# Kernel tuning notes

Hardware: AMD Instinct MI355X
Metric: run time of the kernel (lower is better)

## Reference

```python
import jax, jax.numpy as jnp
import numpy as np

B, N, D, H = 256, 1000, 128, 8
DH = D // H
TANH_CLIP = 10.0
NEG = -1e9  # finite stand-in for -inf mask fill (keeps grads clean)


def setup_inputs() -> dict:
    key = jax.random.key(0)
    ks = jax.random.split(key, 8)
    s = 1.0 / np.sqrt(D)
    return {
        "node_embeddings": jax.random.normal(ks[0], (B, N, D), jnp.float32),
        "W_node": jax.random.normal(ks[1], (D, 3 * D), jnp.float32) * s,   # project_node_embeddings
        "W_fixed": jax.random.normal(ks[2], (D, D), jnp.float32) * s,      # project_fixed_context
        "W_step": jax.random.normal(ks[3], (2 * D, D), jnp.float32) * s,   # project_step_context
        "W_out": jax.random.normal(ks[4], (D, D), jnp.float32) * s,        # project_out
        "prev_idx": jax.random.randint(ks[5], (B,), 0, N),
        "first_idx": jax.random.randint(ks[6], (B,), 0, N),
        "mask": jax.random.randint(ks[7], (B, N), 0, 2).astype(bool),      # True = masked/visited
    }


def reference(node_embeddings, W_node, W_fixed, W_step, W_out, prev_idx, first_idx, mask):
    b = jnp.arange(B)
    # Precompute fixed: context projection of graph embedding (mean aggregation)
    graph_embed = node_embeddings.mean(axis=1)                    # (B, D)
    fixed_context = graph_embed @ W_fixed                          # (B, D)
    # glimpse key / glimpse val / logit key from node embeddings
    kvl = node_embeddings @ W_node                                 # (B, N, 3D)
    glimpse_K, glimpse_V, logit_K = jnp.split(kvl, 3, axis=-1)
    gK = glimpse_K.reshape(B, N, H, DH)                            # (B, N, H, dh)
    gV = glimpse_V.reshape(B, N, H, DH)
    # Step context: cat(first node embed, last node embed) -> query
    step_ctx = jnp.concatenate(
        [node_embeddings[b, first_idx], node_embeddings[b, prev_idx]], axis=-1)  # (B, 2D)
    query = fixed_context + step_ctx @ W_step                      # (B, D)
    Q = query.reshape(B, H, DH)                                    # (B, H, dh)
    # Glimpse MHA (single query per batch element)
    compat = jnp.einsum("bhd,bnhd->bhn", Q, gK) / np.sqrt(DH)      # (B, H, N)
    compat = jnp.where(mask[:, None, :], NEG, compat)              # mask_inner
    attn = jax.nn.softmax(compat, axis=-1)
    heads = jnp.einsum("bhn,bnhd->bhd", attn, gV)                  # (B, H, dh)
    glimpse = heads.reshape(B, D) @ W_out                          # (B, D)
    # Logits against logit_K, tanh clipping, mask_logits, log-softmax
    logits = jnp.einsum("bd,bnd->bn", glimpse, logit_K) / np.sqrt(D)
    logits = TANH_CLIP * jnp.tanh(logits)
    logits = jnp.where(mask, NEG, logits)
    log_p = jax.nn.log_softmax(logits, axis=-1)                    # (B, N)
    return log_p
```

## Files before the change

### kernel.cpp

```cpp
#include <hip/hip_runtime.h>
#include <math.h>

#define BB 256
#define NN 1000
#define DD 128
#define HH 8
#define QQ 4
#define RQ 250
#define NEG -1e9f

#define SY_CNTA 0
#define SY_QK   1
#define SY_CNTC 2
#define SY_GQ   3
#define SY_CNTE 4

__device__ __forceinline__ bool get_mask(const void* m, int flag, size_t idx) {
    if (flag == 1) return ((const int*)m)[idx] != 0;
    if (flag == 2) return ((const float*)m)[idx] != 0.0f;
    return ((const unsigned char*)m)[idx] != 0;
}

__device__ __forceinline__ void sy_arrive(int* p) {
    __builtin_amdgcn_fence(__ATOMIC_RELEASE, "agent");
    __hip_atomic_fetch_add(p, 1, __ATOMIC_RELAXED, __HIP_MEMORY_SCOPE_AGENT);
}
__device__ __forceinline__ void sy_set(int* p) {
    __builtin_amdgcn_fence(__ATOMIC_RELEASE, "agent");
    __hip_atomic_store(p, 1, __ATOMIC_RELAXED, __HIP_MEMORY_SCOPE_AGENT);
}
__device__ __forceinline__ void sy_wait(int* p, int tgt) {
    while (__hip_atomic_load(p, __ATOMIC_RELAXED, __HIP_MEMORY_SCOPE_AGENT) < tgt)
        __builtin_amdgcn_s_sleep(8);
    __builtin_amdgcn_fence(__ATOMIC_ACQUIRE, "agent");
}

__global__ __launch_bounds__(256, 4) void k_one(
        const float* __restrict__ X, const float* __restrict__ Wnode,
        const float* __restrict__ Wfix, const float* __restrict__ Wstep,
        const float* __restrict__ Wout, const int* __restrict__ prev,
        const int* __restrict__ first, const void* __restrict__ mask,
        int* __restrict__ syg, float* __restrict__ partial,
        float* __restrict__ qkg, float* __restrict__ sqw,
        float* __restrict__ pvp, float* __restrict__ gqg,
        float* __restrict__ esumg, float* __restrict__ out) {
    const int bid = blockIdx.x, tid = threadIdx.x;
    const int b = bid >> 2, q = bid & 3;
    const int n0 = q * RQ;
    const size_t xoff = (size_t)b * NN * DD;
    int* sy = syg + b * 16;

    __shared__ __align__(16) unsigned char pool[16384];
    __shared__ __align__(16) float qks[HH][DD];
    __shared__ float gqv[DD];
    __shared__ float lgl[256];
    __shared__ unsigned short cidxL[256];
    __shared__ float redS[4][HH];
    __shared__ float Sh[HH];
    __shared__ float redw[4];
    __shared__ int wbase[4];
    __shared__ int s_flag, s_cnt;
    float* poolf = (float*)pool;

    if (tid < 64) {
        const unsigned int* mw = (const unsigned int*)mask;
        unsigned int a0 = mw[tid], a1 = mw[tid + 64], a2 = mw[tid + 128], a3 = mw[tid + 192];
        int ii = (a0 <= 1u) && (a1 <= 1u) && (a2 <= 1u) && (a3 <= 1u);
        int ff = (a0 == 0u || a0 == 0x3F800000u) && (a1 == 0u || a1 == 0x3F800000u) &&
                 (a2 == 0u || a2 == 0x3F800000u) && (a3 == 0u || a3 == 0x3F800000u);
        int ai = __all(ii), af = __all(ff);
        if (tid == 0) s_flag = ai ? 1 : (af ? 2 : 0);
    }

    {
        float4* red4 = (float4*)pool;
        int c = tid & 31, s = tid >> 5;
        const float4* Xr = (const float4*)(X + xoff);
        float4 acc = make_float4(0.f, 0.f, 0.f, 0.f);
        for (int nl = s; nl < RQ; nl += 8) {
            float4 v = Xr[(n0 + nl) * 32 + c];
            acc.x += v.x; acc.y += v.y; acc.z += v.z; acc.w += v.w;
        }
        red4[s * 32 + c] = acc;
        __syncthreads();
        for (int st = 4; st >= 1; st >>= 1) {
            if (s < st) {
                float4 o = red4[(s + st) * 32 + c];
                float4 r = red4[s * 32 + c];
                r.x += o.x; r.y += o.y; r.z += o.z; r.w += o.w;
                red4[s * 32 + c] = r;
            }
            __syncthreads();
        }
        if (s == 0) {
            float4 r = red4[c];
            float* outp = partial + ((size_t)b * QQ + q) * DD + 4 * c;
            outp[0] = r.x; outp[1] = r.y; outp[2] = r.z; outp[3] = r.w;
        }
    }
    {
        int w = tid >> 6, lane = tid & 63;
        bool un = (tid < RQ) && !get_mask(mask, s_flag, (size_t)b * NN + n0 + tid);
        unsigned long long bal = __ballot(un);
        if (lane == 0) wbase[w] = __popcll(bal);
        __syncthreads();
        int base = 0;
        for (int ww = 0; ww < w; ++ww) base += wbase[ww];
        int off = __popcll(bal & ((1ULL << lane) - 1ULL));
        if (un) cidxL[base + off] = (unsigned short)tid;
        if (tid == 0) s_cnt = wbase[0] + wbase[1] + wbase[2] + wbase[3];
    }
    __syncthreads();
    if (tid == 0) sy_arrive(&sy[SY_CNTA]);

    if (q == 0) {
        if (tid == 0) sy_wait(&sy[SY_CNTA], QQ);
        __syncthreads();
        float* ge = poolf;
        float* sc = poolf + 128;
        float* qv = poolf + 384;
        float* qp = poolf + 512;
        if (tid < DD) {
            float g = 0.f;
            #pragma unroll
            for (int qq = 0; qq < QQ; ++qq) g += partial[((size_t)b * QQ + qq) * DD + tid];
            ge[tid] = g * (1.0f / NN);
        }
        {
            int src = (tid < DD) ? first[b] : prev[b];
            sc[tid] = X[xoff + (size_t)src * DD + (tid & 127)];
        }
        __syncthreads();
        int p = tid >> 7, d = tid & 127;
        {
            float a = 0.f;
            #pragma unroll 4
            for (int k = p * 64; k < p * 64 + 64; ++k)      a += ge[k] * Wfix[(size_t)k * DD + d];
            #pragma unroll 4
            for (int k = p * 128; k < p * 128 + 128; ++k)   a += sc[k] * Wstep[(size_t)k * DD + d];
            qp[p * DD + d] = a;
        }
        __syncthreads();
        if (tid < DD) qv[tid] = qp[tid] + qp[DD + tid];
        __syncthreads();
        {
            const float* wrow = Wnode + (size_t)d * 384;
            #pragma unroll
            for (int h = p * 4; h < p * 4 + 4; ++h) {
                const float4* wr = (const float4*)(wrow + h * 16);
                float a = 0.f;
                #pragma unroll
                for (int j4 = 0; j4 < 4; ++j4) {
                    float4 w = wr[j4];
                    a += w.x * qv[h * 16 + 4 * j4]     + w.y * qv[h * 16 + 4 * j4 + 1]
                       + w.z * qv[h * 16 + 4 * j4 + 2] + w.w * qv[h * 16 + 4 * j4 + 3];
                }
                qkg[((size_t)b * HH + h) * DD + d] = 0.25f * a;
            }
        }
        __syncthreads();
        if (tid == 0) sy_set(&sy[SY_QK]);
    }
    if (tid == 0) sy_wait(&sy[SY_QK], 1);
    __syncthreads();
    for (int i = tid; i < HH * DD; i += 256)
        qks[i >> 7][i & 127] = qkg[(size_t)b * HH * DD + i];
    __syncthreads();

    {
        float* redpv = poolf;
        const int g = tid & 15, r = tid >> 4, w = tid >> 6;
        int len = s_cnt;
        int iters = (len + 15) >> 4;
        float acc[HH][8];
        #pragma unroll
        for (int h = 0; h < HH; ++h)
            #pragma unroll
            for (int j = 0; j < 8; ++j) acc[h][j] = 0.f;
        float S[HH] = {0.f, 0.f, 0.f, 0.f, 0.f, 0.f, 0.f, 0.f};

        for (int it = 0; it < iters; ++it) {
            int k = it * 16 + r;
            if (k < len) {
                int n = n0 + cidxL[k];
                const float4* xr = (const float4*)(X + xoff + (size_t)n * DD + 8 * g);
                float4 v0 = xr[0], v1 = xr[1];
                float v[8] = {v0.x, v0.y, v0.z, v0.w, v1.x, v1.y, v1.z, v1.w};
                float cp[HH];
                #pragma unroll
                for (int h = 0; h < HH; ++h) {
                    const float4* qr = (const float4*)&qks[h][8 * g];
                    float4 q0 = qr[0], q1 = qr[1];
                    cp[h] = v[0] * q0.x + v[1] * q0.y + v[2] * q0.z + v[3] * q0.w
                          + v[4] * q1.x + v[5] * q1.y + v[6] * q1.z + v[7] * q1.w;
                }
                #pragma unroll
                for (int h = 0; h < HH; ++h) {
                    cp[h] += __shfl_xor(cp[h], 1, 16);
                    cp[h] += __shfl_xor(cp[h], 2, 16);
                    cp[h] += __shfl_xor(cp[h], 4, 16);
                    cp[h] += __shfl_xor(cp[h], 8, 16);
                }
                #pragma unroll
                for (int h = 0; h < HH; ++h) {
                    float pe = __expf(fminf(cp[h], 80.f));
                    S[h] += pe;
                    #pragma unroll
                    for (int j = 0; j < 8; ++j) acc[h][j] += pe * v[j];
                }
            }
        }
        #pragma unroll
        for (int h = 0; h < HH; ++h) {
            S[h] += __shfl_xor(S[h], 16, 64);
            S[h] += __shfl_xor(S[h], 32, 64);
            #pragma unroll
            for (int j = 0; j < 8; ++j) {
                acc[h][j] += __shfl_xor(acc[h][j], 16, 64);
                acc[h][j] += __shfl_xor(acc[h][j], 32, 64);
            }
        }
        if ((tid & 63) < 16) {
            #pragma unroll
            for (int h = 0; h < HH; ++h) {
                *((float4*)&redpv[((size_t)w * HH + h) * DD + 8 * g]) =
                    make_float4(acc[h][0], acc[h][1], acc[h][2], acc[h][3]);
                *((float4*)&redpv[((size_t)w * HH + h) * DD + 8 * g + 4]) =
                    make_float4(acc[h][4], acc[h][5], acc[h][6], acc[h][7]);
            }
            if (g == 0) {
                #pragma unroll
                for (int h = 0; h < HH; ++h) redS[w][h] = S[h];
            }
        }
        __syncthreads();
        for (int idx = tid; idx < HH * DD; idx += 256) {
            int h = idx >> 7, d = idx & 127;
            pvp[(((size_t)b * QQ + q) * HH + h) * DD + d] =
                redpv[(0 * HH + h) * DD + d] + redpv[(1 * HH + h) * DD + d] +
                redpv[(2 * HH + h) * DD + d] + redpv[(3 * HH + h) * DD + d];
        }
        if (tid < HH)
            sqw[((size_t)b * QQ + q) * HH + tid] =
                redS[0][tid] + redS[1][tid] + redS[2][tid] + redS[3][tid];
    }
    __syncthreads();
    if (tid == 0) sy_arrive(&sy[SY_CNTC]);

    if (q == 0) {
        if (tid == 0) sy_wait(&sy[SY_CNTC], QQ);
        __syncthreads();
        float* xa = poolf;
        float* hd = poolf + 1024;
        float* gl = poolf + 1152;
        float* qp = poolf + 1280;
        if (tid < HH) {
            float S = 0.f;
            #pragma unroll
            for (int qq = 0; qq < QQ; ++qq) S += sqw[((size_t)b * QQ + qq) * HH + tid];
            Sh[tid] = 1.0f / S;
        }
        __syncthreads();
        for (int idx = tid; idx < HH * DD; idx += 256) {
            int h = idx >> 7, d = idx & 127;
            float a = 0.f;
            #pragma unroll
            for (int qq = 0; qq < QQ; ++qq)
                a += pvp[(((size_t)b * QQ + qq) * HH + h) * DD + d];
            xa[h * DD + d] = a * Sh[h];
        }
        __syncthreads();
        int p = tid >> 7, t = tid & 127;
        {
            int h = t >> 4;
            float a = 0.f;
            #pragma unroll 4
            for (int d = p * 64; d < p * 64 + 64; ++d)
                a += xa[h * DD + d] * Wnode[(size_t)d * 384 + 128 + t];
            qp[p * DD + t] = a;
        }
        __syncthreads();
        if (tid < DD) hd[tid] = qp[tid] + qp[DD + tid];
        __syncthreads();
        {
            float a = 0.f;
            #pragma unroll 4
            for (int k = p * 64; k < p * 64 + 64; ++k) a += hd[k] * Wout[(size_t)k * DD + t];
            qp[p * DD + t] = a;
        }
        __syncthreads();
        if (tid < DD) gl[tid] = qp[tid] + qp[DD + tid];
        __syncthreads();
        {
            const float4* wr = (const float4*)(Wnode + (size_t)t * 384 + 256 + p * 64);
            float a = 0.f;
            #pragma unroll
            for (int j4 = 0; j4 < 16; ++j4) {
                float4 w = wr[j4];
                int k = p * 64 + 4 * j4;
                a += w.x * gl[k] + w.y * gl[k + 1] + w.z * gl[k + 2] + w.w * gl[k + 3];
            }
            qp[p * DD + t] = a;
        }
        __syncthreads();
        if (tid < DD)
            gqg[(size_t)b * DD + tid] = (qp[tid] + qp[DD + tid]) * 0.08838834764831845f;
        __syncthreads();
        if (tid == 0) sy_set(&sy[SY_GQ]);
    }
    if (tid == 0) sy_wait(&sy[SY_GQ], 1);
    __syncthreads();
    if (tid < DD) gqv[tid] = gqg[(size_t)b * DD + tid];
    if (tid < RQ) lgl[tid] = NEG;
    __syncthreads();

    {
        int len = s_cnt;
        int g = tid & 7, rr = tid >> 3;
        int iters = (len + 31) >> 5;
        float esum = 0.f;
        for (int it = 0; it < iters; ++it) {
            int k = it * 32 + rr;
            if (k < len) {
                int nl = cidxL[k];
                const float4* xr = (const float4*)(X + xoff + (size_t)(n0 + nl) * DD);
                float a = 0.f;
                #pragma unroll
                for (int i = 0; i < 4; ++i) {
                    float4 v = xr[g + 8 * i];
                    int col = 4 * (g + 8 * i);
                    a += v.x * gqv[col] + v.y * gqv[col + 1]
                       + v.z * gqv[col + 2] + v.w * gqv[col + 3];
                }
                a += __shfl_xor(a, 1, 8);
                a += __shfl_xor(a, 2, 8);
                a += __shfl_xor(a, 4, 8);
                if (g == 0) {
                    float l = 10.0f * tanhf(a);
                    lgl[nl] = l;
                    esum += __expf(l - 10.0f);
                }
            }
        }
        #pragma unroll
        for (int off = 32; off >= 1; off >>= 1) esum += __shfl_xor(esum, off, 64);
        if ((tid & 63) == 0) redw[tid >> 6] = esum;
        __syncthreads();
        if (tid == 0) esumg[(size_t)b * QQ + q] = redw[0] + redw[1] + redw[2] + redw[3];
    }
    __syncthreads();
    if (tid == 0) { sy_arrive(&sy[SY_CNTE]); sy_wait(&sy[SY_CNTE], QQ); }
    __syncthreads();

    {
        float s = esumg[(size_t)b * QQ] + esumg[(size_t)b * QQ + 1]
                + esumg[(size_t)b * QQ + 2] + esumg[(size_t)b * QQ + 3];
        float lse = 10.0f + logf(s);
        if (tid < RQ) out[(size_t)b * NN + n0 + tid] = lgl[tid] - lse;
    }
}

__global__ __launch_bounds__(1024) void k_mega(
        const float* __restrict__ X, const float* __restrict__ Wnode,
        const float* __restrict__ Wfix, const float* __restrict__ Wstep,
        const float* __restrict__ Wout, const int* __restrict__ prev,
        const int* __restrict__ first, const void* __restrict__ mask,
        float* __restrict__ out) {
    int b = blockIdx.x, tid = threadIdx.x;
    __shared__ __align__(16) float cm[HH * 1024];
    __shared__ __align__(16) float qkl[HH * DD];
    __shared__ __align__(16) float qpart[8 * DD];
    __shared__ float xa[HH * DD];
    __shared__ float ge[DD], q[DD], sc[2 * DD], hd[DD], gl[DD], gqv[DD];
    __shared__ float red[16], invh[8];
    __shared__ int s_flag;
    const size_t xoff = (size_t)b * NN * DD;

    if (tid < 64) {
        const unsigned int* mw = (const unsigned int*)mask;
        unsigned int a0 = mw[tid], a1 = mw[tid + 64], a2 = mw[tid + 128], a3 = mw[tid + 192];
        int ii = (a0 <= 1u) && (a1 <= 1u) && (a2 <= 1u) && (a3 <= 1u);
        int ff = (a0 == 0u || a0 == 0x3F800000u) && (a1 == 0u || a1 == 0x3F800000u) &&
                 (a2 == 0u || a2 == 0x3F800000u) && (a3 == 0u || a3 == 0x3F800000u);
        int ai = __all(ii), af = __all(ff);
        if (tid == 0) s_flag = ai ? 1 : (af ? 2 : 0);
    }
    if (tid >= 256 && tid < 512) {
        int t = tid - 256;
        int src = (t < DD) ? first[b] : prev[b];
        sc[t] = X[xoff + (size_t)src * DD + (t & 127)];
    }
    {
        float4* red4 = (float4*)cm;
        int c = tid & 31, s = tid >> 5;
        const float4* Xr = (const float4*)(X + xoff);
        float4 acc = make_float4(0.f, 0.f, 0.f, 0.f);
        for (int n = s; n < NN; n += 32) {
            float4 v = Xr[n * 32 + c];
            acc.x += v.x; acc.y += v.y; acc.z += v.z; acc.w += v.w;
        }
        red4[s * 32 + c] = acc;
        __syncthreads();
        for (int st = 16; st >= 1; st >>= 1) {
            if (s < st) {
                float4 o = red4[(s + st) * 32 + c];
                float4 r = red4[s * 32 + c];
                r.x += o.x; r.y += o.y; r.z += o.z; r.w += o.w;
                red4[s * 32 + c] = r;
            }
            __syncthreads();
        }
        if (s == 0) {
            float4 r = red4[c];
            ge[4 * c] = r.x * (1.0f / NN); ge[4 * c + 1] = r.y * (1.0f / NN);
            ge[4 * c + 2] = r.z * (1.0f / NN); ge[4 * c + 3] = r.w * (1.0f / NN);
        }
        __syncthreads();
    }
    const int flag = s_flag;
    {
        int p = tid >> 7, d = tid & 127;
        float a = 0.f;
        for (int k = p * 16; k < p * 16 + 16; ++k) a += ge[k] * Wfix[k * DD + d];
        for (int k = p * 32; k < p * 32 + 32; ++k) a += sc[k] * Wstep[k * DD + d];
        qpart[p * DD + d] = a;
        __syncthreads();
        if (tid < DD) {
            float s = 0.f;
            for (int pp = 0; pp < 8; ++pp) s += qpart[pp * DD + tid];
            q[tid] = s;
        }
        __syncthreads();
        int d2 = tid >> 3, h = tid & 7;
        const float4* wr = (const float4*)(Wnode + (size_t)d2 * 384 + h * 16);
        float a2 = 0.f;
        for (int j4 = 0; j4 < 4; ++j4) {
            float4 w = wr[j4];
            a2 += w.x * q[h * 16 + 4 * j4]     + w.y * q[h * 16 + 4 * j4 + 1]
                + w.z * q[h * 16 + 4 * j4 + 2] + w.w * q[h * 16 + 4 * j4 + 3];
        }
        qkl[h * DD + d2] = 0.25f * a2;
        __syncthreads();
    }
    {
        int g = tid & 7;
        for (int it = 0; it < 8; ++it) {
            int n = it * 128 + (tid >> 3);
            if (n < NN) {
                float acc[HH] = {0.f, 0.f, 0.f, 0.f, 0.f, 0.f, 0.f, 0.f};
                const float4* xr = (const float4*)(X + xoff + (size_t)n * DD);
                for (int i = 0; i < 4; ++i) {
                    float4 v = xr[g + 8 * i];
                    int col = 4 * (g + 8 * i);
                    for (int h = 0; h < HH; ++h)
                        acc[h] += v.x * qkl[h * DD + col]     + v.y * qkl[h * DD + col + 1]
                                + v.z * qkl[h * DD + col + 2] + v.w * qkl[h * DD + col + 3];
                }
                for (int h = 0; h < HH; ++h) {
                    acc[h] += __shfl_xor(acc[h], 1, 8);
                    acc[h] += __shfl_xor(acc[h], 2, 8);
                    acc[h] += __shfl_xor(acc[h], 4, 8);
                }
                float val = acc[0];
                for (int h = 1; h < HH; ++h) val = (g == h) ? acc[h] : val;
                bool mk = get_mask(mask, flag, (size_t)b * NN + n);
                cm[g * 1024 + n] = mk ? NEG : val;
            }
        }
        __syncthreads();
    }
    {
        int h = tid >> 7, lane = tid & 127;
        float mx = -INFINITY;
        for (int n = lane; n < NN; n += 128) mx = fmaxf(mx, cm[h * 1024 + n]);
        for (int off = 32; off >= 1; off >>= 1) mx = fmaxf(mx, __shfl_xor(mx, off, 64));
        if ((tid & 63) == 0) red[tid >> 6] = mx;
        __syncthreads();
        float m_h = fmaxf(red[2 * h], red[2 * h + 1]);
        float sm = 0.f;
        for (int n = lane; n < NN; n += 128) {
            float p = __expf(cm[h * 1024 + n] - m_h);
            cm[h * 1024 + n] = p;
            sm += p;
        }
        for (int off = 32; off >= 1; off >>= 1) sm += __shfl_xor(sm, off, 64);
        __syncthreads();
        if ((tid & 63) == 0) red[tid >> 6] = sm;
        __syncthreads();
        if (tid < HH) invh[tid] = 1.0f / (red[2 * tid] + red[2 * tid + 1]);
        __syncthreads();
    }
    {
        int s = tid >> 7, d = tid & 127;
        float acc[HH] = {0.f, 0.f, 0.f, 0.f, 0.f, 0.f, 0.f, 0.f};
        for (int n = s; n < NN; n += 8) {
            float x = X[xoff + (size_t)n * DD + d];
            for (int h = 0; h < HH; ++h) acc[h] += cm[h * 1024 + n] * x;
        }
        __syncthreads();
        float* xp = cm;
        for (int h = 0; h < HH; ++h) xp[(s * HH + h) * DD + d] = acc[h];
        __syncthreads();
        if (s == 0) {
            for (int h = 0; h < HH; ++h) {
                float t = 0.f;
                for (int ss = 0; ss < 8; ++ss) t += xp[(ss * HH + h) * DD + d];
                xa[h * DD + d] = t * invh[h];
            }
        }
        __syncthreads();
    }
    {
        int p = tid >> 7, t = tid & 127;
        int h = t >> 4;
        float a = 0.f;
        for (int d = p * 16; d < p * 16 + 16; ++d)
            a += xa[h * DD + d] * Wnode[(size_t)d * 384 + 128 + t];
        qpart[p * DD + t] = a;
        __syncthreads();
        if (tid < DD) {
            float s = 0.f;
            for (int pp = 0; pp < 8; ++pp) s += qpart[pp * DD + tid];
            hd[tid] = s;
        }
        __syncthreads();
        a = 0.f;
        for (int k = p * 16; k < p * 16 + 16; ++k) a += hd[k] * Wout[(size_t)k * DD + t];
        qpart[p * DD + t] = a;
        __syncthreads();
        if (tid < DD) {
            float s = 0.f;
            for (int pp = 0; pp < 8; ++pp) s += qpart[pp * DD + tid];
            gl[tid] = s;
        }
        __syncthreads();
        const float4* wr = (const float4*)(Wnode + (size_t)t * 384 + 256 + p * 16);
        a = 0.f;
        for (int j4 = 0; j4 < 4; ++j4) {
            float4 w = wr[j4];
            int k = p * 16 + 4 * j4;
            a += w.x * gl[k] + w.y * gl[k + 1] + w.z * gl[k + 2] + w.w * gl[k + 3];
        }
        qpart[p * DD + t] = a;
        __syncthreads();
        if (tid < DD) {
            float s = 0.f;
            for (int pp = 0; pp < 8; ++pp) s += qpart[pp * DD + tid];
            gqv[tid] = s * 0.08838834764831845f;
        }
        __syncthreads();
    }
    {
        float* lg = qkl;
        int g = tid & 7;
        for (int it = 0; it < 8; ++it) {
            int n = it * 128 + (tid >> 3);
            if (n < NN) {
                const float4* xr = (const float4*)(X + xoff + (size_t)n * DD);
                float a = 0.f;
                for (int i = 0; i < 4; ++i) {
                    float4 v = xr[g + 8 * i];
                    int col = 4 * (g + 8 * i);
                    a += v.x * gqv[col] + v.y * gqv[col + 1] + v.z * gqv[col + 2] + v.w * gqv[col + 3];
                }
                a += __shfl_xor(a, 1, 8);
                a += __shfl_xor(a, 2, 8);
                a += __shfl_xor(a, 4, 8);
                if (g == 0) {
                    float lgt = 10.0f * tanhf(a);
                    lg[n] = get_mask(mask, flag, (size_t)b * NN + n) ? NEG : lgt;
                }
            }
        }
        __syncthreads();
        float v = (tid < NN) ? lg[tid] : -INFINITY;
        float mx = v;
        for (int off = 32; off >= 1; off >>= 1) mx = fmaxf(mx, __shfl_xor(mx, off, 64));
        if ((tid & 63) == 0) red[tid >> 6] = mx;
        __syncthreads();
        float m = red[0];
        for (int w = 1; w < 16; ++w) m = fmaxf(m, red[w]);
        float e = (tid < NN) ? __expf(v - m) : 0.f;
        float sm = e;
        for (int off = 32; off >= 1; off >>= 1) sm += __shfl_xor(sm, off, 64);
        __syncthreads();
        if ((tid & 63) == 0) red[tid >> 6] = sm;
        __syncthreads();
        float s2 = 0.f;
        for (int w = 0; w < 16; ++w) s2 += red[w];
        float lse = m + logf(s2);
        if (tid < NN) out[(size_t)b * NN + tid] = v - lse;
    }
}

extern "C" void kernel_launch(void* const* d_in, const int* in_sizes, int n_in,
                              void* d_out, int out_size, void* d_ws, size_t ws_size,
                              hipStream_t stream) {
    const float* X     = (const float*)d_in[0];
    const float* Wnode = (const float*)d_in[1];
    const float* Wfix  = (const float*)d_in[2];
    const float* Wstep = (const float*)d_in[3];
    const float* Wout  = (const float*)d_in[4];
    const int*   prev  = (const int*)d_in[5];
    const int*   first = (const int*)d_in[6];
    const void*  mask  = d_in[7];
    float* out = (float*)d_out;

    char* wsb = (char*)d_ws;
    int*   syg     = (int*)wsb;
    float* partial = (float*)(wsb + 16384);
    float* qkg     = partial + (size_t)BB * QQ * DD;
    float* sqw     = qkg + (size_t)BB * HH * DD;
    float* pvp     = sqw + (size_t)BB * QQ * HH;
    float* gqg     = pvp + (size_t)BB * QQ * HH * DD;
    float* esumg   = gqg + (size_t)BB * DD;
    const size_t need = 16384 + sizeof(float) * (
        (size_t)BB * QQ * DD + (size_t)BB * HH * DD + (size_t)BB * QQ * HH +
        (size_t)BB * QQ * HH * DD + (size_t)BB * DD + (size_t)BB * QQ);

    int maxb = 0;
    bool ok = (ws_size >= need) &&
              (hipOccupancyMaxActiveBlocksPerMultiprocessor(&maxb, (const void*)k_one,
                                                            256, 0) == hipSuccess) &&
              (maxb >= QQ);
    if (ok) {
        hipMemsetAsync(syg, 0, 16384, stream);
        k_one<<<BB * QQ, 256, 0, stream>>>(X, Wnode, Wfix, Wstep, Wout, prev, first,
                                           mask, syg, partial, qkg, sqw, pvp, gqg,
                                           esumg, out);
    } else {
        k_mega<<<BB, 1024, 0, stream>>>(X, Wnode, Wfix, Wstep, Wout,
                                        prev, first, mask, out);
    }
}
```

Measured before the change: 107.5 us.

## Compute query projections redundantly per block to drop leader-broadcast syncs

Each of the four blocks serving one batch element now computes the query-key and glimpse-query projections itself, instead of block 0 computing them and publishing them through global memory behind set/wait flags. This removes two serial leader phases and their global round-trips, at the cost of four times the small matvec work and weight reads. The attention loop is also reshaped to 32 lanes per row with float4 loads and fewer accumulators, and both loops are made branch-free via clamped indices. Some unroll factors are raised.

```diff
diff --git a/kernel.cpp b/kernel.cpp
--- a/kernel.cpp
+++ b/kernel.cpp
@@ -10,10 +10,8 @@
 #define NEG -1e9f
 
 #define SY_CNTA 0
-#define SY_QK   1
-#define SY_CNTC 2
-#define SY_GQ   3
-#define SY_CNTE 4
+#define SY_CNTC 1
+#define SY_CNTE 2
 
 __device__ __forceinline__ bool get_mask(const void* m, int flag, size_t idx) {
     if (flag == 1) return ((const int*)m)[idx] != 0;
@@ -21,18 +19,15 @@
     return ((const unsigned char*)m)[idx] != 0;
 }
 
-__device__ __forceinline__ void sy_arrive(int* p) {
-    __builtin_amdgcn_fence(__ATOMIC_RELEASE, "agent");
-    __hip_atomic_fetch_add(p, 1, __ATOMIC_RELAXED, __HIP_MEMORY_SCOPE_AGENT);
-}
-__device__ __forceinline__ void sy_set(int* p) {
-    __builtin_amdgcn_fence(__ATOMIC_RELEASE, "agent");
-    __hip_atomic_store(p, 1, __ATOMIC_RELAXED, __HIP_MEMORY_SCOPE_AGENT);
-}
-__device__ __forceinline__ void sy_wait(int* p, int tgt) {
-    while (__hip_atomic_load(p, __ATOMIC_RELAXED, __HIP_MEMORY_SCOPE_AGENT) < tgt)
-        __builtin_amdgcn_s_sleep(8);
-    __builtin_amdgcn_fence(__ATOMIC_ACQUIRE, "agent");
+__device__ __forceinline__ void sy_barrier(int* p, int tid, int tgt) {
+    if (tid == 0) {
+        __builtin_amdgcn_fence(__ATOMIC_RELEASE, "agent");
+        __hip_atomic_fetch_add(p, 1, __ATOMIC_RELAXED, __HIP_MEMORY_SCOPE_AGENT);
+        while (__hip_atomic_load(p, __ATOMIC_RELAXED, __HIP_MEMORY_SCOPE_AGENT) < tgt)
+            __builtin_amdgcn_s_sleep(8);
+        __builtin_amdgcn_fence(__ATOMIC_ACQUIRE, "agent");
+    }
+    __syncthreads();
 }
 
 __global__ __launch_bounds__(256, 4) void k_one(
@@ -41,8 +36,7 @@
         const float* __restrict__ Wout, const int* __restrict__ prev,
         const int* __restrict__ first, const void* __restrict__ mask,
         int* __restrict__ syg, float* __restrict__ partial,
-        float* __restrict__ qkg, float* __restrict__ sqw,
-        float* __restrict__ pvp, float* __restrict__ gqg,
+        float* __restrict__ sqw, float* __restrict__ pvp,
         float* __restrict__ esumg, float* __restrict__ out) {
     const int bid = blockIdx.x, tid = threadIdx.x;
     const int b = bid >> 2, q = bid & 3;
@@ -50,7 +44,7 @@
     const size_t xoff = (size_t)b * NN * DD;
     int* sy = syg + b * 16;
 
-    __shared__ __align__(16) unsigned char pool[16384];
+    __shared__ __align__(16) float pool[4096];
     __shared__ __align__(16) float qks[HH][DD];
     __shared__ float gqv[DD];
     __shared__ float lgl[256];
@@ -60,7 +54,6 @@
     __shared__ float redw[4];
     __shared__ int wbase[4];
     __shared__ int s_flag, s_cnt;
-    float* poolf = (float*)pool;
 
     if (tid < 64) {
         const unsigned int* mw = (const unsigned int*)mask;
@@ -111,15 +104,13 @@
         if (tid == 0) s_cnt = wbase[0] + wbase[1] + wbase[2] + wbase[3];
     }
     __syncthreads();
-    if (tid == 0) sy_arrive(&sy[SY_CNTA]);
-
-    if (q == 0) {
-        if (tid == 0) sy_wait(&sy[SY_CNTA], QQ);
-        __syncthreads();
-        float* ge = poolf;
-        float* sc = poolf + 128;
-        float* qv = poolf + 384;
-        float* qp = poolf + 512;
+    sy_barrier(&sy[SY_CNTA], tid, QQ);
+
+    {
+        float* ge = pool;
+        float* sc = pool + 128;
+        float* qv = pool + 384;
+        float* qp = pool + 512;
         if (tid < DD) {
             float g = 0.f;
             #pragma unroll
@@ -134,9 +125,9 @@
         int p = tid >> 7, d = tid & 127;
         {
             float a = 0.f;
-            #pragma unroll 4
+            #pragma unroll 8
             for (int k = p * 64; k < p * 64 + 64; ++k)      a += ge[k] * Wfix[(size_t)k * DD + d];
-            #pragma unroll 4
+            #pragma unroll 8
             for (int k = p * 128; k < p * 128 + 128; ++k)   a += sc[k] * Wstep[(size_t)k * DD + d];
             qp[p * DD + d] = a;
         }
@@ -155,79 +146,65 @@
                     a += w.x * qv[h * 16 + 4 * j4]     + w.y * qv[h * 16 + 4 * j4 + 1]
                        + w.z * qv[h * 16 + 4 * j4 + 2] + w.w * qv[h * 16 + 4 * j4 + 3];
                 }
-                qkg[((size_t)b * HH + h) * DD + d] = 0.25f * a;
-            }
-        }
-        __syncthreads();
-        if (tid == 0) sy_set(&sy[SY_QK]);
-    }
-    if (tid == 0) sy_wait(&sy[SY_QK], 1);
-    __syncthreads();
-    for (int i = tid; i < HH * DD; i += 256)
-        qks[i >> 7][i & 127] = qkg[(size_t)b * HH * DD + i];
-    __syncthreads();
-
-    {
-        float* redpv = poolf;
-        const int g = tid & 15, r = tid >> 4, w = tid >> 6;
-        int len = s_cnt;
-        int iters = (len + 15) >> 4;
-        float acc[HH][8];
-        #pragma unroll
-        for (int h = 0; h < HH; ++h)
-            #pragma unroll
-            for (int j = 0; j < 8; ++j) acc[h][j] = 0.f;
-        float S[HH] = {0.f, 0.f, 0.f, 0.f, 0.f, 0.f, 0.f, 0.f};
-
-        for (int it = 0; it < iters; ++it) {
-            int k = it * 16 + r;
-            if (k < len) {
-                int n = n0 + cidxL[k];
-                const float4* xr = (const float4*)(X + xoff + (size_t)n * DD + 8 * g);
-                float4 v0 = xr[0], v1 = xr[1];
-                float v[8] = {v0.x, v0.y, v0.z, v0.w, v1.x, v1.y, v1.z, v1.w};
-                float cp[HH];
-                #pragma unroll
-                for (int h = 0; h < HH; ++h) {
-                    const float4* qr = (const float4*)&qks[h][8 * g];
-                    float4 q0 = qr[0], q1 = qr[1];
-                    cp[h] = v[0] * q0.x + v[1] * q0.y + v[2] * q0.z + v[3] * q0.w
-                          + v[4] * q1.x + v[5] * q1.y + v[6] * q1.z + v[7] * q1.w;
-                }
-                #pragma unroll
-                for (int h = 0; h < HH; ++h) {
-                    cp[h] += __shfl_xor(cp[h], 1, 16);
-                    cp[h] += __shfl_xor(cp[h], 2, 16);
-                    cp[h] += __shfl_xor(cp[h], 4, 16);
-                    cp[h] += __shfl_xor(cp[h], 8, 16);
-                }
-                #pragma unroll
-                for (int h = 0; h < HH; ++h) {
-                    float pe = __expf(fminf(cp[h], 80.f));
-                    S[h] += pe;
-                    #pragma unroll
-                    for (int j = 0; j < 8; ++j) acc[h][j] += pe * v[j];
-                }
-            }
-        }
+                qks[h][d] = 0.25f * a;
+            }
+        }
+        __syncthreads();
+    }
+
+    {
+        float* redpv = pool;
+        const int g = tid & 31, r = tid >> 5, w = tid >> 6;
+        const int len = s_cnt;
+        const int iters = (len + 7) >> 3;
+        float acc[HH][4];
         #pragma unroll
         for (int h = 0; h < HH; ++h) {
-            S[h] += __shfl_xor(S[h], 16, 64);
+            acc[h][0] = 0.f; acc[h][1] = 0.f; acc[h][2] = 0.f; acc[h][3] = 0.f;
+        }
+        float S[HH] = {0.f, 0.f, 0.f, 0.f, 0.f, 0.f, 0.f, 0.f};
+
+        for (int it = 0; it < iters; ++it) {
+            int k = it * 8 + r;
+            bool valid = (k < len);
+            int kk = valid ? k : (len - 1);
+            int n = n0 + cidxL[kk];
+            float4 v = *(const float4*)(X + xoff + (size_t)n * DD + 4 * g);
+            float cp[HH];
+            #pragma unroll
+            for (int h = 0; h < HH; ++h) {
+                cp[h] = v.x * qks[h][4 * g]     + v.y * qks[h][4 * g + 1]
+                      + v.z * qks[h][4 * g + 2] + v.w * qks[h][4 * g + 3];
+            }
+            #pragma unroll
+            for (int h = 0; h < HH; ++h) {
+                cp[h] += __shfl_xor(cp[h], 1, 32);
+                cp[h] += __shfl_xor(cp[h], 2, 32);
+                cp[h] += __shfl_xor(cp[h], 4, 32);
+                cp[h] += __shfl_xor(cp[h], 8, 32);
+                cp[h] += __shfl_xor(cp[h], 16, 32);
+            }
+            #pragma unroll
+            for (int h = 0; h < HH; ++h) {
+                float pe = valid ? __expf(fminf(cp[h], 80.f)) : 0.f;
+                S[h] += pe;
+                acc[h][0] += pe * v.x; acc[h][1] += pe * v.y;
+                acc[h][2] += pe * v.z; acc[h][3] += pe * v.w;
+            }
+        }
+        #pragma unroll
+        for (int h = 0; h < HH; ++h) {
             S[h] += __shfl_xor(S[h], 32, 64);
-            #pragma unroll
-            for (int j = 0; j < 8; ++j) {
-                acc[h][j] += __shfl_xor(acc[h][j], 16, 64);
-                acc[h][j] += __shfl_xor(acc[h][j], 32, 64);
-            }
-        }
-        if ((tid & 63) < 16) {
-            #pragma unroll
-            for (int h = 0; h < HH; ++h) {
-                *((float4*)&redpv[((size_t)w * HH + h) * DD + 8 * g]) =
+            acc[h][0] += __shfl_xor(acc[h][0], 32, 64);
+            acc[h][1] += __shfl_xor(acc[h][1], 32, 64);
+            acc[h][2] += __shfl_xor(acc[h][2], 32, 64);
+            acc[h][3] += __shfl_xor(acc[h][3], 32, 64);
+        }
+        if ((tid & 63) < 32) {
+            #pragma unroll
+            for (int h = 0; h < HH; ++h)
+                *((float4*)&redpv[((size_t)w * HH + h) * DD + 4 * g]) =
                     make_float4(acc[h][0], acc[h][1], acc[h][2], acc[h][3]);
-                *((float4*)&redpv[((size_t)w * HH + h) * DD + 8 * g + 4]) =
-                    make_float4(acc[h][4], acc[h][5], acc[h][6], acc[h][7]);
-            }
             if (g == 0) {
                 #pragma unroll
                 for (int h = 0; h < HH; ++h) redS[w][h] = S[h];
@@ -245,21 +222,20 @@
                 redS[0][tid] + redS[1][tid] + redS[2][tid] + redS[3][tid];
     }
     __syncthreads();
-    if (tid == 0) sy_arrive(&sy[SY_CNTC]);
-
-    if (q == 0) {
-        if (tid == 0) sy_wait(&sy[SY_CNTC], QQ);
-        __syncthreads();
-        float* xa = poolf;
-        float* hd = poolf + 1024;
-        float* gl = poolf + 1152;
-        float* qp = poolf + 1280;
+    sy_barrier(&sy[SY_CNTC], tid, QQ);
+
+    {
+        float* xa = pool;
+        float* hd = pool + 1024;
+        float* gl = pool + 1152;
+        float* qp = pool + 1280;
         if (tid < HH) {
             float S = 0.f;
             #pragma unroll
             for (int qq = 0; qq < QQ; ++qq) S += sqw[((size_t)b * QQ + qq) * HH + tid];
             Sh[tid] = 1.0f / S;
         }
+        if (tid < RQ) lgl[tid] = NEG;
         __syncthreads();
         for (int idx = tid; idx < HH * DD; idx += 256) {
             int h = idx >> 7, d = idx & 127;
@@ -274,7 +250,7 @@
         {
             int h = t >> 4;
             float a = 0.f;
-            #pragma unroll 4
+            #pragma unroll 8
             for (int d = p * 64; d < p * 64 + 64; ++d)
                 a += xa[h * DD + d] * Wnode[(size_t)d * 384 + 128 + t];
             qp[p * DD + t] = a;
@@ -284,7 +260,7 @@
         __syncthreads();
         {
             float a = 0.f;
-            #pragma unroll 4
+            #pragma unroll 8
             for (int k = p * 64; k < p * 64 + 64; ++k) a += hd[k] * Wout[(size_t)k * DD + t];
             qp[p * DD + t] = a;
         }
@@ -303,43 +279,36 @@
             qp[p * DD + t] = a;
         }
         __syncthreads();
-        if (tid < DD)
-            gqg[(size_t)b * DD + tid] = (qp[tid] + qp[DD + tid]) * 0.08838834764831845f;
-        __syncthreads();
-        if (tid == 0) sy_set(&sy[SY_GQ]);
-    }
-    if (tid == 0) sy_wait(&sy[SY_GQ], 1);
-    __syncthreads();
-    if (tid < DD) gqv[tid] = gqg[(size_t)b * DD + tid];
-    if (tid < RQ) lgl[tid] = NEG;
-    __syncthreads();
-
-    {
-        int len = s_cnt;
+        if (tid < DD) gqv[tid] = (qp[tid] + qp[DD + tid]) * 0.08838834764831845f;
+        __syncthreads();
+    }
+
+    {
+        const int len = s_cnt;
+        const int iters = (len + 31) >> 5;
         int g = tid & 7, rr = tid >> 3;
-        int iters = (len + 31) >> 5;
         float esum = 0.f;
         for (int it = 0; it < iters; ++it) {
             int k = it * 32 + rr;
-            if (k < len) {
-                int nl = cidxL[k];
-                const float4* xr = (const float4*)(X + xoff + (size_t)(n0 + nl) * DD);
-                float a = 0.f;
-                #pragma unroll
-                for (int i = 0; i < 4; ++i) {
-                    float4 v = xr[g + 8 * i];
-                    int col = 4 * (g + 8 * i);
-                    a += v.x * gqv[col] + v.y * gqv[col + 1]
-                       + v.z * gqv[col + 2] + v.w * gqv[col + 3];
-                }
-                a += __shfl_xor(a, 1, 8);
-                a += __shfl_xor(a, 2, 8);
-                a += __shfl_xor(a, 4, 8);
-                if (g == 0) {
-                    float l = 10.0f * tanhf(a);
-                    lgl[nl] = l;
-                    esum += __expf(l - 10.0f);
-                }
+            bool valid = (k < len);
+            int kk = valid ? k : (len - 1);
+            int nl = cidxL[kk];
+            const float4* xr = (const float4*)(X + xoff + (size_t)(n0 + nl) * DD);
+            float a = 0.f;
+            #pragma unroll
+            for (int i = 0; i < 4; ++i) {
+                float4 v = xr[g + 8 * i];
+                int col = 4 * (g + 8 * i);
+                a += v.x * gqv[col] + v.y * gqv[col + 1]
+                   + v.z * gqv[col + 2] + v.w * gqv[col + 3];
+            }
+            a += __shfl_xor(a, 1, 8);
+            a += __shfl_xor(a, 2, 8);
+            a += __shfl_xor(a, 4, 8);
+            if (g == 0 && valid) {
+                float l = 10.0f * tanhf(a);
+                lgl[nl] = l;
+                esum += __expf(l - 10.0f);
             }
         }
         #pragma unroll
@@ -349,8 +318,7 @@
         if (tid == 0) esumg[(size_t)b * QQ + q] = redw[0] + redw[1] + redw[2] + redw[3];
     }
     __syncthreads();
-    if (tid == 0) { sy_arrive(&sy[SY_CNTE]); sy_wait(&sy[SY_CNTE], QQ); }
-    __syncthreads();
+    sy_barrier(&sy[SY_CNTE], tid, QQ);
 
     {
         float s = esumg[(size_t)b * QQ] + esumg[(size_t)b * QQ + 1]
@@ -609,14 +577,12 @@
     char* wsb = (char*)d_ws;
     int*   syg     = (int*)wsb;
     float* partial = (float*)(wsb + 16384);
-    float* qkg     = partial + (size_t)BB * QQ * DD;
-    float* sqw     = qkg + (size_t)BB * HH * DD;
+    float* sqw     = partial + (size_t)BB * QQ * DD;
     float* pvp     = sqw + (size_t)BB * QQ * HH;
-    float* gqg     = pvp + (size_t)BB * QQ * HH * DD;
-    float* esumg   = gqg + (size_t)BB * DD;
+    float* esumg   = pvp + (size_t)BB * QQ * HH * DD;
     const size_t need = 16384 + sizeof(float) * (
-        (size_t)BB * QQ * DD + (size_t)BB * HH * DD + (size_t)BB * QQ * HH +
-        (size_t)BB * QQ * HH * DD + (size_t)BB * DD + (size_t)BB * QQ);
+        (size_t)BB * QQ * DD + (size_t)BB * QQ * HH +
+        (size_t)BB * QQ * HH * DD + (size_t)BB * QQ);
 
     int maxb = 0;
     bool ok = (ws_size >= need) &&
@@ -626,8 +592,7 @@
     if (ok) {
         hipMemsetAsync(syg, 0, 16384, stream);
         k_one<<<BB * QQ, 256, 0, stream>>>(X, Wnode, Wfix, Wstep, Wout, prev, first,
-                                           mask, syg, partial, qkg, sqw, pvp, gqg,
-                                           esumg, out);
+                                           mask, syg, partial, sqw, pvp, esumg, out);
     } else {
         k_mega<<<BB, 1024, 0, stream>>>(X, Wnode, Wfix, Wstep, Wout,
                                         prev, first, mask, out);
```

After: 107.2 us. About the same (-0.3%).
